# Performance work log

Hardware: AMD Instinct MI355X
Metric: run time of the kernel (lower is better)

## Reference

```python
import jax, jax.numpy as jnp
import numpy as np


def ternarize_weight(w):
    # abs-mean threshold quantization to {-am, 0, +am}
    abs_mean = jnp.maximum(jnp.abs(w).mean(), 1e-5)
    thr = 0.7 * abs_mean
    q = jnp.where(w > thr, 1.0, jnp.where(w < -thr, -1.0, 0.0))
    # STE: forward value is q*abs_mean, grad flows to w as identity
    return w + jax.lax.stop_gradient(q * abs_mean - w)


def rotate_half(x):
    x1, x2 = jnp.split(x, 2, axis=-1)
    return jnp.concatenate([-x2, x1], axis=-1)


def setup_inputs() -> dict:
    key = jax.random.key(0)
    k1, k2, k3, k4, k5 = jax.random.split(key, 5)
    B, T, C, H = 2, 2048, 1024, 16
    D = C // H
    x = jax.random.normal(k1, (B, T, C), dtype=jnp.float32)
    cos = jax.random.uniform(k2, (1, 1, T, D), dtype=jnp.float32)
    sin = jax.random.uniform(k3, (1, 1, T, D), dtype=jnp.float32)
    w_qkv = jax.random.normal(k4, (3 * C, C), dtype=jnp.float32) / np.sqrt(C)
    w_proj = jax.random.normal(k5, (C, C), dtype=jnp.float32) / np.sqrt(C)
    return {"x": x, "cos": cos, "sin": sin, "w_qkv": w_qkv, "w_proj": w_proj}


def reference(x, cos, sin, w_qkv, w_proj):
    B, T, C = x.shape
    H = 16
    D = C // H
    wq = ternarize_weight(w_qkv)
    wp = ternarize_weight(w_proj)
    qkv = x @ wq.T  # [B,T,3C]
    q, k, v = jnp.split(qkv, 3, axis=-1)
    # [B,T,C] -> [B,H,T,D]
    q = q.reshape(B, T, H, D).transpose(0, 2, 1, 3)
    k = k.reshape(B, T, H, D).transpose(0, 2, 1, 3)
    v = v.reshape(B, T, H, D).transpose(0, 2, 1, 3)
    # RoPE
    q = q * cos + rotate_half(q) * sin
    k = k * cos + rotate_half(k) * sin
    # causal SDPA
    scale = 1.0 / np.sqrt(D)
    scores = jnp.einsum("bhqd,bhkd->bhqk", q, k) * scale
    causal = jnp.tril(jnp.ones((T, T), dtype=bool))
    scores = jnp.where(causal, scores, jnp.finfo(scores.dtype).min)
    attn = jax.nn.softmax(scores, axis=-1)
    y = jnp.einsum("bhqk,bhkd->bhqd", attn, v)  # [B,H,T,D]
    y = y.transpose(0, 2, 1, 3).reshape(B, T, C)
    return y @ wp.T
```

## Files before the change

kernel.cpp:

```cpp
#include <hip/hip_runtime.h>
#include <hip/hip_bf16.h>

#define B_ 2
#define T_ 2048
#define C_ 1024
#define H_ 16
#define D_ 64
#define M_ 4096
#define N3C 3072

using short8  = __attribute__((ext_vector_type(8))) short;
using floatx4 = __attribute__((ext_vector_type(4))) float;
typedef unsigned int u32;

__device__ __forceinline__ unsigned short f2b(float f) {
  __hip_bfloat16 h = __float2bfloat16(f);
  return *reinterpret_cast<unsigned short*>(&h);
}
__device__ __forceinline__ float b2f(unsigned short u) {
  union { unsigned int i; float f; } x; x.i = ((unsigned int)u) << 16; return x.f;
}

__device__ __forceinline__ void gll16(const void* g, void* l) {
  __builtin_amdgcn_global_load_lds((const __attribute__((address_space(1))) u32*)g,
                                   (__attribute__((address_space(3))) u32*)l, 16, 0, 0);
}


__global__ void zero_sums(double* sums) {
  if (threadIdx.x < 2) sums[threadIdx.x] = 0.0;
}

__global__ void abs_sum_kernel(const float* __restrict__ w, int n4, double* out) {
  __shared__ double red[4];
  int stride = gridDim.x * blockDim.x;
  double s = 0.0;
  for (int i = blockIdx.x * blockDim.x + threadIdx.x; i < n4; i += stride) {
    float4 v = ((const float4*)w)[i];
    s += (double)fabsf(v.x) + (double)fabsf(v.y) + (double)fabsf(v.z) + (double)fabsf(v.w);
  }
  #pragma unroll
  for (int off = 32; off > 0; off >>= 1)
    s += __shfl_down(s, off, 64);
  if ((threadIdx.x & 63) == 0) red[threadIdx.x >> 6] = s;
  __syncthreads();
  if (threadIdx.x == 0) atomicAdd(out, (red[0] + red[1]) + (red[2] + red[3]));
}

__global__ void ternarize_all(const float* __restrict__ wq, const float* __restrict__ wp,
                              unsigned short* __restrict__ oq, unsigned short* __restrict__ op,
                              const double* __restrict__ sums, float* __restrict__ ams) {
  const int NQ = 3 * C_ * C_;
  const int NP = C_ * C_;
  int i = blockIdx.x * blockDim.x + threadIdx.x;
  float am0 = fmaxf((float)(sums[0] * (1.0 / NQ)), 1e-5f);
  float am1 = fmaxf((float)(sums[1] * (1.0 / NP)), 1e-5f);
  if (i == 0) { ams[0] = am0; ams[1] = am1; }
  if (i < NQ) {
    float thr = 0.7f * am0, x = wq[i];
    oq[i] = (x > thr) ? 0x3F80u : ((x < -thr) ? 0xBF80u : 0u);
  } else if (i < NQ + NP) {
    int j = i - NQ;
    float thr = 0.7f * am1, x = wp[j];
    op[j] = (x > thr) ? 0x3F80u : ((x < -thr) ? 0xBF80u : 0u);
  }
}

__global__ void cvt_f32_bf16(const float* __restrict__ in, unsigned short* __restrict__ out, int n4) {
  int i = blockIdx.x * blockDim.x + threadIdx.x;
  if (i < n4) {
    float4 v = ((const float4*)in)[i];
    ushort4 o; o.x = f2b(v.x); o.y = f2b(v.y); o.z = f2b(v.z); o.w = f2b(v.w);
    ((ushort4*)out)[i] = o;
  }
}


template<int OUT_BF16>
__global__ __launch_bounds__(256) void gemm128(const unsigned short* __restrict__ A,
                                               const unsigned short* __restrict__ W,
                                               const float* __restrict__ scale_ptr,
                                               void* __restrict__ Cout,
                                               int N, int K) {
  __shared__ __attribute__((aligned(16))) unsigned short As[128 * 32];
  __shared__ __attribute__((aligned(16))) unsigned short Ws[128 * 32];
  const int tid = threadIdx.x, lane = tid & 63, wv = tid >> 6;
  const int m = lane & 15, g = lane >> 4;
  const int m0 = blockIdx.y * 128, n0 = blockIdx.x * 128;
  const int wm = (wv >> 1) * 64, wn = (wv & 1) * 64;

  const int srow = wv * 16 + (lane >> 2);
  const int skoff = (lane & 3) * 8;
  const unsigned short* ga0 = A + (size_t)(m0 + srow) * K + skoff;
  const unsigned short* ga1 = A + (size_t)(m0 + 64 + srow) * K + skoff;
  const unsigned short* gw0 = W + (size_t)(n0 + srow) * K + skoff;
  const unsigned short* gw1 = W + (size_t)(n0 + 64 + srow) * K + skoff;
  unsigned short* la0 = As + (wv * 16) * 32;
  unsigned short* la1 = As + (64 + wv * 16) * 32;
  unsigned short* lw0 = Ws + (wv * 16) * 32;
  unsigned short* lw1 = Ws + (64 + wv * 16) * 32;

  floatx4 acc[4][4] = {};
  for (int kc = 0; kc < K; kc += 32) {
    __syncthreads();
    gll16(ga0, la0); gll16(ga1, la1); gll16(gw0, lw0); gll16(gw1, lw1);
    ga0 += 32; ga1 += 32; gw0 += 32; gw1 += 32;
    __syncthreads();
    short8 af[4], wf[4];
    #pragma unroll
    for (int r = 0; r < 4; r++)
      af[r] = *(const short8*)&As[(wm + r * 16 + m) * 32 + g * 8];
    #pragma unroll
    for (int c = 0; c < 4; c++)
      wf[c] = *(const short8*)&Ws[(wn + c * 16 + m) * 32 + g * 8];
    #pragma unroll
    for (int r = 0; r < 4; r++)
      #pragma unroll
      for (int c = 0; c < 4; c++)
        acc[r][c] = __builtin_amdgcn_mfma_f32_16x16x32_bf16(af[r], wf[c], acc[r][c], 0, 0, 0);
  }

  const float scale = *scale_ptr;
  #pragma unroll
  for (int r = 0; r < 4; r++)
    #pragma unroll
    for (int c = 0; c < 4; c++)
      #pragma unroll
      for (int i = 0; i < 4; i++) {
        int row = m0 + wm + r * 16 + g * 4 + i;
        int col = n0 + wn + c * 16 + m;
        float val = acc[r][c][i] * scale;
        if (OUT_BF16) ((unsigned short*)Cout)[(size_t)row * N + col] = f2b(val);
        else          ((float*)Cout)[(size_t)row * N + col] = val;
      }
}


__global__ __launch_bounds__(256) void rope_vtrans(const unsigned short* __restrict__ qkv,
                                                   const float* __restrict__ cosp,
                                                   const float* __restrict__ sinp,
                                                   unsigned short* __restrict__ Qb,
                                                   unsigned short* __restrict__ Kb,
                                                   unsigned short* __restrict__ Vtb) {
  __shared__ unsigned short L[64][65];
  const float QSC = 0.125f * 1.44269504088896340736f;
  const int bh = blockIdx.y, t0 = blockIdx.x * 64;
  const int b = bh >> 4, h = bh & 15;
  const size_t hb = (size_t)bh * T_ * 64;
  #pragma unroll
  for (int it = 0; it < 8; it++) {
    int idx = it * 256 + threadIdx.x;
    int tl = idx >> 5, p = idx & 31, t = t0 + tl;
    size_t rb = (size_t)(b * T_ + t) * N3C + h * 64;
    float q1 = b2f(qkv[rb + p]),      q2 = b2f(qkv[rb + p + 32]);
    float k1 = b2f(qkv[rb + C_ + p]), k2 = b2f(qkv[rb + C_ + p + 32]);
    float c1 = cosp[t * 64 + p], c2 = cosp[t * 64 + p + 32];
    float s1 = sinp[t * 64 + p], s2 = sinp[t * 64 + p + 32];
    size_t ob = hb + (size_t)t * 64;
    Qb[ob + p]      = f2b((q1 * c1 - q2 * s1) * QSC);
    Qb[ob + p + 32] = f2b((q2 * c2 + q1 * s2) * QSC);
    Kb[ob + p]      = f2b(k1 * c1 - k2 * s1);
    Kb[ob + p + 32] = f2b(k2 * c2 + k1 * s2);
  }
  #pragma unroll
  for (int it = 0; it < 16; it++) {
    int idx = it * 256 + threadIdx.x;
    int tl = idx >> 6, d = idx & 63;
    L[tl][d] = qkv[(size_t)(b * T_ + t0 + tl) * N3C + 2 * C_ + h * 64 + d];
  }
  __syncthreads();
  #pragma unroll
  for (int it = 0; it < 16; it++) {
    int idx = it * 256 + threadIdx.x;
    int dr = idx >> 6, tl = idx & 63;
    Vtb[hb + (size_t)dr * T_ + t0 + tl] = L[tl][dr];
  }
}


__global__ __launch_bounds__(256) void flash_mfma(const unsigned short* __restrict__ Qb,
                                                  const unsigned short* __restrict__ Kb,
                                                  const unsigned short* __restrict__ Vtb,
                                                  unsigned short* __restrict__ Y) {
  __shared__ __align__(16) unsigned short Ktile[2][64][64];
  __shared__ __align__(16) unsigned short Vtile[2][64][64];
  __shared__ __align__(16) unsigned short Plds[4][16][72];
  const int lane = threadIdx.x & 63;
  const int wv = threadIdx.x >> 6;
  const int m = lane & 15, g = lane >> 4;
  const int gid = blockIdx.x;
  const int xcd = gid & 7, idx = gid >> 3;
  const int bh = xcd * 4 + (idx >> 3);
  const int pr = idx & 7;
  const int b = bh >> 4, h = bh & 15;
  const size_t hb = (size_t)bh * T_ * 64;
  const unsigned short* Kbh = Kb + hb;
  const unsigned short* Vbh = Vtb + hb;
  const int r8 = lane >> 3, cc8 = lane & 7;
  const int gcol = ((cc8 ^ r8) << 3);

  #pragma unroll
  for (int sp = 0; sp < 2; sp++) {
    const int s = sp ? (15 - pr) : pr;
    const int ntiles = 2 * s + 2;
    const int qb0 = s * 128 + wv * 32;
    const int qb1 = qb0 + 16;

    const unsigned short* qp0 = Qb + hb + (size_t)(qb0 + m) * 64 + g * 8;
    short8 qf00 = *(const short8*)qp0;
    short8 qf01 = *(const short8*)(qp0 + 32);
    const unsigned short* qp1 = qp0 + 16 * 64;
    short8 qf10 = *(const short8*)qp1;
    short8 qf11 = *(const short8*)(qp1 + 32);

    floatx4 O0[4] = {}, O1[4] = {};
    float ls0 = 0.f, ls1 = 0.f;

    if (sp) __syncthreads();
    #pragma unroll
    for (int cc = 0; cc < 2; cc++) {
      int row = wv * 16 + cc * 8;
      gll16(Kbh + (size_t)(row + r8) * 64 + gcol, &Ktile[0][row][0]);
      gll16(Vbh + (size_t)(row + r8) * T_ + gcol, &Vtile[0][row][0]);
    }

    for (int kt = 0; kt < ntiles; kt++) {
      const int buf = kt & 1;
      const int kb = kt * 64;
      __syncthreads();
      if (kt + 1 < ntiles) {
        const int kb2 = kb + 64;
        #pragma unroll
        for (int cc = 0; cc < 2; cc++) {
          int row = wv * 16 + cc * 8;
          gll16(Kbh + (size_t)(kb2 + row + r8) * 64 + gcol, &Ktile[1 - buf][row][0]);
          gll16(Vbh + (size_t)(row + r8) * T_ + kb2 + gcol, &Vtile[1 - buf][row][0]);
        }
      }
      if (kb > qb0 + 31) continue;

      auto do_qset = [&](short8 qa, short8 qb_, int qbase, float& lsum, floatx4* O) {
        floatx4 S[4];
        #pragma unroll
        for (int mt = 0; mt < 4; mt++) {
          int row = mt * 16 + m;
          short8 kf0 = *(const short8*)&Ktile[buf][row][(g ^ (m & 7)) << 3];
          short8 kf1 = *(const short8*)&Ktile[buf][row][((g + 4) ^ (m & 7)) << 3];
          floatx4 sv = {};
          sv = __builtin_amdgcn_mfma_f32_16x16x32_bf16(kf0, qa, sv, 0, 0, 0);
          sv = __builtin_amdgcn_mfma_f32_16x16x32_bf16(kf1, qb_, sv, 0, 0, 0);
          S[mt] = sv;
        }
        if (kb + 64 <= qbase) {
          #pragma unroll
          for (int mt = 0; mt < 4; mt++) {
            float e0 = exp2f(S[mt][0]), e1 = exp2f(S[mt][1]);
            float e2 = exp2f(S[mt][2]), e3 = exp2f(S[mt][3]);
            lsum += (e0 + e1) + (e2 + e3);
            ushort4 o; o.x = f2b(e0); o.y = f2b(e1); o.z = f2b(e2); o.w = f2b(e3);
            *(ushort4*)&Plds[wv][m][mt * 16 + g * 4] = o;
          }
        } else {
          const int q_glob = qbase + m;
          #pragma unroll
          for (int mt = 0; mt < 4; mt++) {
            float e[4];
            #pragma unroll
            for (int r = 0; r < 4; r++) {
              int kg = kb + mt * 16 + g * 4 + r;
              e[r] = (kg <= q_glob) ? exp2f(S[mt][r]) : 0.f;
            }
            lsum += (e[0] + e[1]) + (e[2] + e[3]);
            ushort4 o; o.x = f2b(e[0]); o.y = f2b(e[1]); o.z = f2b(e[2]); o.w = f2b(e[3]);
            *(ushort4*)&Plds[wv][m][mt * 16 + g * 4] = o;
          }
        }
        short8 pa0 = *(const short8*)&Plds[wv][m][g * 8];
        short8 pa1 = *(const short8*)&Plds[wv][m][32 + g * 8];
        #pragma unroll
        for (int nt = 0; nt < 4; nt++) {
          int row = nt * 16 + m;
          short8 v0 = *(const short8*)&Vtile[buf][row][(g ^ (m & 7)) << 3];
          short8 v1 = *(const short8*)&Vtile[buf][row][((g + 4) ^ (m & 7)) << 3];
          O[nt] = __builtin_amdgcn_mfma_f32_16x16x32_bf16(pa0, v0, O[nt], 0, 0, 0);
          O[nt] = __builtin_amdgcn_mfma_f32_16x16x32_bf16(pa1, v1, O[nt], 0, 0, 0);
        }
      };

      do_qset(qf00, qf01, qb0, ls0, O0);
      if (kb <= qb1 + 15) do_qset(qf10, qf11, qb1, ls1, O1);
    }

    #pragma unroll
    for (int j = 0; j < 2; j++) {
      float lsum = j ? ls1 : ls0;
      floatx4* O = j ? O1 : O0;
      const int qbase = j ? qb1 : qb0;
      lsum += __shfl_xor(lsum, 16, 64);
      lsum += __shfl_xor(lsum, 32, 64);
      float li[4];
      #pragma unroll
      for (int r = 0; r < 4; r++) li[r] = 1.0f / __shfl(lsum, g * 4 + r, 64);
      #pragma unroll
      for (int nt = 0; nt < 4; nt++)
        #pragma unroll
        for (int r = 0; r < 4; r++) {
          int trow = qbase + g * 4 + r;
          int col = h * 64 + nt * 16 + m;
          Y[(size_t)(b * T_ + trow) * C_ + col] = f2b(O[nt][r] * li[r]);
        }
    }
  }
}


extern "C" void kernel_launch(void* const* d_in, const int* in_sizes, int n_in,
                              void* d_out, int out_size, void* d_ws, size_t ws_size,
                              hipStream_t stream) {
  (void)in_sizes; (void)n_in; (void)out_size; (void)ws_size;
  const float* x      = (const float*)d_in[0];
  const float* cosp   = (const float*)d_in[1];
  const float* sinp   = (const float*)d_in[2];
  const float* w_qkv  = (const float*)d_in[3];
  const float* w_proj = (const float*)d_in[4];
  float* out = (float*)d_out;

  char* ws = (char*)d_ws;
  double* sums = (double*)ws;
  float*  ams  = (float*)(ws + 16);
  unsigned short* wqkv_b  = (unsigned short*)(ws + 256);
  unsigned short* wproj_b = wqkv_b + (size_t)N3C * C_;
  unsigned short* xb      = wproj_b + (size_t)C_ * C_;
  unsigned short* qkv_b   = xb + (size_t)M_ * C_;
  unsigned short* Qb      = qkv_b + (size_t)M_ * N3C;
  unsigned short* Kb      = Qb + (size_t)B_ * H_ * T_ * D_;
  unsigned short* Vtb     = Kb + (size_t)B_ * H_ * T_ * D_;
  unsigned short* yb      = Vtb + (size_t)B_ * H_ * T_ * D_;

  zero_sums<<<1, 64, 0, stream>>>(sums);
  abs_sum_kernel<<<256, 256, 0, stream>>>(w_qkv, (3 * C_ * C_) / 4, sums + 0);
  abs_sum_kernel<<<128, 256, 0, stream>>>(w_proj, (C_ * C_) / 4, sums + 1);
  ternarize_all<<<(4 * C_ * C_) / 256, 256, 0, stream>>>(w_qkv, w_proj, wqkv_b, wproj_b,
                                                         sums, ams);
  cvt_f32_bf16<<<(M_ * C_ / 4 + 255) / 256, 256, 0, stream>>>(x, xb, M_ * C_ / 4);
  gemm128<1><<<dim3(N3C / 128, M_ / 128), 256, 0, stream>>>(xb, wqkv_b, ams + 0, qkv_b, N3C, C_);
  rope_vtrans<<<dim3(T_ / 64, B_ * H_), 256, 0, stream>>>(qkv_b, cosp, sinp, Qb, Kb, Vtb);
  flash_mfma<<<256, 256, 0, stream>>>(Qb, Kb, Vtb, yb);
  gemm128<0><<<dim3(C_ / 128, M_ / 128), 256, 0, stream>>>(yb, wproj_b, ams + 1, out, C_, C_);
}
```

Before: 224.3 us.

## Fuse RoPE into QKV GEMM epilogue, merge abs-sum launches, and re-split flash blocks

The QKV GEMM epilogue now applies RoPE and scaling and writes Q, K and V directly in head-major layout, which removes the separate qkv round trip through memory. The old rope kernel is reduced to a V transpose only. The two abs-sum launches become one 2D launch. Flash attention now runs 512 blocks that each handle one 64-row query tile per wave set with paired causal tiles, where before each block handled two 16-row q-sets per wave. This raises parallelism but drops the per-wave double q-set reuse of K/V tiles.

```diff
diff --git a/kernel.cpp b/kernel.cpp
--- a/kernel.cpp
+++ b/kernel.cpp
@@ -31,8 +31,11 @@
   if (threadIdx.x < 2) sums[threadIdx.x] = 0.0;
 }
 
-__global__ void abs_sum_kernel(const float* __restrict__ w, int n4, double* out) {
+__global__ void abs_sum2(const float* __restrict__ wq, const float* __restrict__ wp,
+                         double* __restrict__ sums) {
   __shared__ double red[4];
+  const float* w = blockIdx.y ? wp : wq;
+  const int n4 = blockIdx.y ? (C_ * C_ / 4) : (3 * C_ * C_ / 4);
   int stride = gridDim.x * blockDim.x;
   double s = 0.0;
   for (int i = blockIdx.x * blockDim.x + threadIdx.x; i < n4; i += stride) {
@@ -44,7 +47,7 @@
     s += __shfl_down(s, off, 64);
   if ((threadIdx.x & 63) == 0) red[threadIdx.x >> 6] = s;
   __syncthreads();
-  if (threadIdx.x == 0) atomicAdd(out, (red[0] + red[1]) + (red[2] + red[3]));
+  if (threadIdx.x == 0) atomicAdd(sums + blockIdx.y, (red[0] + red[1]) + (red[2] + red[3]));
 }
 
 __global__ void ternarize_all(const float* __restrict__ wq, const float* __restrict__ wp,
@@ -76,12 +79,15 @@
 }
 
 
-template<int OUT_BF16>
-__global__ __launch_bounds__(256) void gemm128(const unsigned short* __restrict__ A,
-                                               const unsigned short* __restrict__ W,
-                                               const float* __restrict__ scale_ptr,
-                                               void* __restrict__ Cout,
-                                               int N, int K) {
+__global__ __launch_bounds__(256) void gemm_qkv(const unsigned short* __restrict__ A,
+                                                const unsigned short* __restrict__ W,
+                                                const float* __restrict__ scale_ptr,
+                                                const float* __restrict__ cosp,
+                                                const float* __restrict__ sinp,
+                                                unsigned short* __restrict__ Qb,
+                                                unsigned short* __restrict__ Kb,
+                                                unsigned short* __restrict__ Vb) {
+  const int K = C_;
   __shared__ __attribute__((aligned(16))) unsigned short As[128 * 32];
   __shared__ __attribute__((aligned(16))) unsigned short Ws[128 * 32];
   const int tid = threadIdx.x, lane = tid & 63, wv = tid >> 6;
@@ -120,6 +126,88 @@
         acc[r][c] = __builtin_amdgcn_mfma_f32_16x16x32_bf16(af[r], wf[c], acc[r][c], 0, 0, 0);
   }
 
+  const float am = *scale_ptr;
+  const int sect = n0 >> 10;
+  const int nloc = n0 & 1023;
+  const int h = (nloc + wn) >> 6;
+  if (sect < 2) {
+    unsigned short* dst = sect ? Kb : Qb;
+    const float sc = sect ? am : am * 0.18033688011112042f;
+    #pragma unroll
+    for (int r = 0; r < 4; r++)
+      #pragma unroll
+      for (int i = 0; i < 4; i++) {
+        int row = m0 + wm + r * 16 + g * 4 + i;
+        int t = row & (T_ - 1), b = row >> 11;
+        size_t obase = ((size_t)(b * H_ + h) * T_ + t) * 64;
+        #pragma unroll
+        for (int c = 0; c < 4; c++) {
+          int p = c * 16 + m;
+          float cv = cosp[t * 64 + p], sv = sinp[t * 64 + p];
+          float a = acc[r][c][i], pt = acc[r][c ^ 2][i];
+          float val = (c < 2) ? (a * cv - pt * sv) : (a * cv + pt * sv);
+          dst[obase + p] = f2b(val * sc);
+        }
+      }
+  } else {
+    #pragma unroll
+    for (int r = 0; r < 4; r++)
+      #pragma unroll
+      for (int i = 0; i < 4; i++) {
+        int row = m0 + wm + r * 16 + g * 4 + i;
+        int t = row & (T_ - 1), b = row >> 11;
+        size_t obase = ((size_t)(b * H_ + h) * T_ + t) * 64;
+        #pragma unroll
+        for (int c = 0; c < 4; c++)
+          Vb[obase + c * 16 + m] = f2b(acc[r][c][i] * am);
+      }
+  }
+}
+
+
+__global__ __launch_bounds__(256) void gemm128(const unsigned short* __restrict__ A,
+                                               const unsigned short* __restrict__ W,
+                                               const float* __restrict__ scale_ptr,
+                                               float* __restrict__ Cout,
+                                               int N, int K) {
+  __shared__ __attribute__((aligned(16))) unsigned short As[128 * 32];
+  __shared__ __attribute__((aligned(16))) unsigned short Ws[128 * 32];
+  const int tid = threadIdx.x, lane = tid & 63, wv = tid >> 6;
+  const int m = lane & 15, g = lane >> 4;
+  const int m0 = blockIdx.y * 128, n0 = blockIdx.x * 128;
+  const int wm = (wv >> 1) * 64, wn = (wv & 1) * 64;
+
+  const int srow = wv * 16 + (lane >> 2);
+  const int skoff = (lane & 3) * 8;
+  const unsigned short* ga0 = A + (size_t)(m0 + srow) * K + skoff;
+  const unsigned short* ga1 = A + (size_t)(m0 + 64 + srow) * K + skoff;
+  const unsigned short* gw0 = W + (size_t)(n0 + srow) * K + skoff;
+  const unsigned short* gw1 = W + (size_t)(n0 + 64 + srow) * K + skoff;
+  unsigned short* la0 = As + (wv * 16) * 32;
+  unsigned short* la1 = As + (64 + wv * 16) * 32;
+  unsigned short* lw0 = Ws + (wv * 16) * 32;
+  unsigned short* lw1 = Ws + (64 + wv * 16) * 32;
+
+  floatx4 acc[4][4] = {};
+  for (int kc = 0; kc < K; kc += 32) {
+    __syncthreads();
+    gll16(ga0, la0); gll16(ga1, la1); gll16(gw0, lw0); gll16(gw1, lw1);
+    ga0 += 32; ga1 += 32; gw0 += 32; gw1 += 32;
+    __syncthreads();
+    short8 af[4], wf[4];
+    #pragma unroll
+    for (int r = 0; r < 4; r++)
+      af[r] = *(const short8*)&As[(wm + r * 16 + m) * 32 + g * 8];
+    #pragma unroll
+    for (int c = 0; c < 4; c++)
+      wf[c] = *(const short8*)&Ws[(wn + c * 16 + m) * 32 + g * 8];
+    #pragma unroll
+    for (int r = 0; r < 4; r++)
+      #pragma unroll
+      for (int c = 0; c < 4; c++)
+        acc[r][c] = __builtin_amdgcn_mfma_f32_16x16x32_bf16(af[r], wf[c], acc[r][c], 0, 0, 0);
+  }
+
   const float scale = *scale_ptr;
   #pragma unroll
   for (int r = 0; r < 4; r++)
@@ -129,44 +217,21 @@
       for (int i = 0; i < 4; i++) {
         int row = m0 + wm + r * 16 + g * 4 + i;
         int col = n0 + wn + c * 16 + m;
-        float val = acc[r][c][i] * scale;
-        if (OUT_BF16) ((unsigned short*)Cout)[(size_t)row * N + col] = f2b(val);
-        else          ((float*)Cout)[(size_t)row * N + col] = val;
-      }
-}
-
-
-__global__ __launch_bounds__(256) void rope_vtrans(const unsigned short* __restrict__ qkv,
-                                                   const float* __restrict__ cosp,
-                                                   const float* __restrict__ sinp,
-                                                   unsigned short* __restrict__ Qb,
-                                                   unsigned short* __restrict__ Kb,
+        Cout[(size_t)row * N + col] = acc[r][c][i] * scale;
+      }
+}
+
+
+__global__ __launch_bounds__(256) void v_transpose(const unsigned short* __restrict__ Vb,
                                                    unsigned short* __restrict__ Vtb) {
   __shared__ unsigned short L[64][65];
-  const float QSC = 0.125f * 1.44269504088896340736f;
   const int bh = blockIdx.y, t0 = blockIdx.x * 64;
-  const int b = bh >> 4, h = bh & 15;
   const size_t hb = (size_t)bh * T_ * 64;
-  #pragma unroll
-  for (int it = 0; it < 8; it++) {
-    int idx = it * 256 + threadIdx.x;
-    int tl = idx >> 5, p = idx & 31, t = t0 + tl;
-    size_t rb = (size_t)(b * T_ + t) * N3C + h * 64;
-    float q1 = b2f(qkv[rb + p]),      q2 = b2f(qkv[rb + p + 32]);
-    float k1 = b2f(qkv[rb + C_ + p]), k2 = b2f(qkv[rb + C_ + p + 32]);
-    float c1 = cosp[t * 64 + p], c2 = cosp[t * 64 + p + 32];
-    float s1 = sinp[t * 64 + p], s2 = sinp[t * 64 + p + 32];
-    size_t ob = hb + (size_t)t * 64;
-    Qb[ob + p]      = f2b((q1 * c1 - q2 * s1) * QSC);
-    Qb[ob + p + 32] = f2b((q2 * c2 + q1 * s2) * QSC);
-    Kb[ob + p]      = f2b(k1 * c1 - k2 * s1);
-    Kb[ob + p + 32] = f2b(k2 * c2 + k1 * s2);
-  }
   #pragma unroll
   for (int it = 0; it < 16; it++) {
     int idx = it * 256 + threadIdx.x;
     int tl = idx >> 6, d = idx & 63;
-    L[tl][d] = qkv[(size_t)(b * T_ + t0 + tl) * N3C + 2 * C_ + h * 64 + d];
+    L[tl][d] = Vb[hb + (size_t)(t0 + tl) * 64 + d];
   }
   __syncthreads();
   #pragma unroll
@@ -189,9 +254,9 @@
   const int wv = threadIdx.x >> 6;
   const int m = lane & 15, g = lane >> 4;
   const int gid = blockIdx.x;
-  const int xcd = gid & 7, idx = gid >> 3;
-  const int bh = xcd * 4 + (idx >> 3);
-  const int pr = idx & 7;
+  const int xcd = gid & 7, j = gid >> 3;
+  const int bh = xcd * 4 + (j >> 4);
+  const int pr = j & 15;
   const int b = bh >> 4, h = bh & 15;
   const size_t hb = (size_t)bh * T_ * 64;
   const unsigned short* Kbh = Kb + hb;
@@ -201,20 +266,17 @@
 
   #pragma unroll
   for (int sp = 0; sp < 2; sp++) {
-    const int s = sp ? (15 - pr) : pr;
-    const int ntiles = 2 * s + 2;
-    const int qb0 = s * 128 + wv * 32;
-    const int qb1 = qb0 + 16;
-
-    const unsigned short* qp0 = Qb + hb + (size_t)(qb0 + m) * 64 + g * 8;
-    short8 qf00 = *(const short8*)qp0;
-    short8 qf01 = *(const short8*)(qp0 + 32);
-    const unsigned short* qp1 = qp0 + 16 * 64;
-    short8 qf10 = *(const short8*)qp1;
-    short8 qf11 = *(const short8*)(qp1 + 32);
-
-    floatx4 O0[4] = {}, O1[4] = {};
-    float ls0 = 0.f, ls1 = 0.f;
+    const int s = sp ? pr : (31 - pr);
+    const int qbase = s * 64 + wv * 16;
+    const int q_glob = qbase + m;
+    const int ntiles = s + 1;
+
+    const unsigned short* qp = Qb + hb + (size_t)(qbase + m) * 64 + g * 8;
+    short8 qf0 = *(const short8*)qp;
+    short8 qf1 = *(const short8*)(qp + 32);
+
+    floatx4 O[4] = {};
+    float lsum = 0.f;
 
     if (sp) __syncthreads();
     #pragma unroll
@@ -237,79 +299,65 @@
           gll16(Vbh + (size_t)(row + r8) * T_ + kb2 + gcol, &Vtile[1 - buf][row][0]);
         }
       }
-      if (kb > qb0 + 31) continue;
-
-      auto do_qset = [&](short8 qa, short8 qb_, int qbase, float& lsum, floatx4* O) {
-        floatx4 S[4];
+      floatx4 S[4];
+      #pragma unroll
+      for (int mt = 0; mt < 4; mt++) {
+        int row = mt * 16 + m;
+        short8 kf0 = *(const short8*)&Ktile[buf][row][(g ^ (m & 7)) << 3];
+        short8 kf1 = *(const short8*)&Ktile[buf][row][((g + 4) ^ (m & 7)) << 3];
+        floatx4 sv = {};
+        sv = __builtin_amdgcn_mfma_f32_16x16x32_bf16(kf0, qf0, sv, 0, 0, 0);
+        sv = __builtin_amdgcn_mfma_f32_16x16x32_bf16(kf1, qf1, sv, 0, 0, 0);
+        S[mt] = sv;
+      }
+      if (kt + 1 < ntiles) {
         #pragma unroll
         for (int mt = 0; mt < 4; mt++) {
-          int row = mt * 16 + m;
-          short8 kf0 = *(const short8*)&Ktile[buf][row][(g ^ (m & 7)) << 3];
-          short8 kf1 = *(const short8*)&Ktile[buf][row][((g + 4) ^ (m & 7)) << 3];
-          floatx4 sv = {};
-          sv = __builtin_amdgcn_mfma_f32_16x16x32_bf16(kf0, qa, sv, 0, 0, 0);
-          sv = __builtin_amdgcn_mfma_f32_16x16x32_bf16(kf1, qb_, sv, 0, 0, 0);
-          S[mt] = sv;
+          float e0 = exp2f(S[mt][0]), e1 = exp2f(S[mt][1]);
+          float e2 = exp2f(S[mt][2]), e3 = exp2f(S[mt][3]);
+          lsum += (e0 + e1) + (e2 + e3);
+          ushort4 o; o.x = f2b(e0); o.y = f2b(e1); o.z = f2b(e2); o.w = f2b(e3);
+          *(ushort4*)&Plds[wv][m][mt * 16 + g * 4] = o;
         }
-        if (kb + 64 <= qbase) {
+      } else {
+        #pragma unroll
+        for (int mt = 0; mt < 4; mt++) {
+          float e[4];
           #pragma unroll
-          for (int mt = 0; mt < 4; mt++) {
-            float e0 = exp2f(S[mt][0]), e1 = exp2f(S[mt][1]);
-            float e2 = exp2f(S[mt][2]), e3 = exp2f(S[mt][3]);
-            lsum += (e0 + e1) + (e2 + e3);
-            ushort4 o; o.x = f2b(e0); o.y = f2b(e1); o.z = f2b(e2); o.w = f2b(e3);
-            *(ushort4*)&Plds[wv][m][mt * 16 + g * 4] = o;
+          for (int r = 0; r < 4; r++) {
+            int kg = kb + mt * 16 + g * 4 + r;
+            e[r] = (kg <= q_glob) ? exp2f(S[mt][r]) : 0.f;
           }
-        } else {
-          const int q_glob = qbase + m;
-          #pragma unroll
-          for (int mt = 0; mt < 4; mt++) {
-            float e[4];
-            #pragma unroll
-            for (int r = 0; r < 4; r++) {
-              int kg = kb + mt * 16 + g * 4 + r;
-              e[r] = (kg <= q_glob) ? exp2f(S[mt][r]) : 0.f;
-            }
-            lsum += (e[0] + e[1]) + (e[2] + e[3]);
-            ushort4 o; o.x = f2b(e[0]); o.y = f2b(e[1]); o.z = f2b(e[2]); o.w = f2b(e[3]);
-            *(ushort4*)&Plds[wv][m][mt * 16 + g * 4] = o;
-          }
+          lsum += (e[0] + e[1]) + (e[2] + e[3]);
+          ushort4 o; o.x = f2b(e[0]); o.y = f2b(e[1]); o.z = f2b(e[2]); o.w = f2b(e[3]);
+          *(ushort4*)&Plds[wv][m][mt * 16 + g * 4] = o;
         }
-        short8 pa0 = *(const short8*)&Plds[wv][m][g * 8];
-        short8 pa1 = *(const short8*)&Plds[wv][m][32 + g * 8];
-        #pragma unroll
-        for (int nt = 0; nt < 4; nt++) {
-          int row = nt * 16 + m;
-          short8 v0 = *(const short8*)&Vtile[buf][row][(g ^ (m & 7)) << 3];
-          short8 v1 = *(const short8*)&Vtile[buf][row][((g + 4) ^ (m & 7)) << 3];
-          O[nt] = __builtin_amdgcn_mfma_f32_16x16x32_bf16(pa0, v0, O[nt], 0, 0, 0);
-          O[nt] = __builtin_amdgcn_mfma_f32_16x16x32_bf16(pa1, v1, O[nt], 0, 0, 0);
-        }
-      };
-
-      do_qset(qf00, qf01, qb0, ls0, O0);
-      if (kb <= qb1 + 15) do_qset(qf10, qf11, qb1, ls1, O1);
+      }
+      short8 pa0 = *(const short8*)&Plds[wv][m][g * 8];
+      short8 pa1 = *(const short8*)&Plds[wv][m][32 + g * 8];
+      #pragma unroll
+      for (int nt = 0; nt < 4; nt++) {
+        int row = nt * 16 + m;
+        short8 v0 = *(const short8*)&Vtile[buf][row][(g ^ (m & 7)) << 3];
+        short8 v1 = *(const short8*)&Vtile[buf][row][((g + 4) ^ (m & 7)) << 3];
+        O[nt] = __builtin_amdgcn_mfma_f32_16x16x32_bf16(pa0, v0, O[nt], 0, 0, 0);
+        O[nt] = __builtin_amdgcn_mfma_f32_16x16x32_bf16(pa1, v1, O[nt], 0, 0, 0);
+      }
     }
 
-    #pragma unroll
-    for (int j = 0; j < 2; j++) {
-      float lsum = j ? ls1 : ls0;
-      floatx4* O = j ? O1 : O0;
-      const int qbase = j ? qb1 : qb0;
-      lsum += __shfl_xor(lsum, 16, 64);
-      lsum += __shfl_xor(lsum, 32, 64);
-      float li[4];
-      #pragma unroll
-      for (int r = 0; r < 4; r++) li[r] = 1.0f / __shfl(lsum, g * 4 + r, 64);
-      #pragma unroll
-      for (int nt = 0; nt < 4; nt++)
-        #pragma unroll
-        for (int r = 0; r < 4; r++) {
-          int trow = qbase + g * 4 + r;
-          int col = h * 64 + nt * 16 + m;
-          Y[(size_t)(b * T_ + trow) * C_ + col] = f2b(O[nt][r] * li[r]);
-        }
-    }
+    lsum += __shfl_xor(lsum, 16, 64);
+    lsum += __shfl_xor(lsum, 32, 64);
+    float li[4];
+    #pragma unroll
+    for (int r = 0; r < 4; r++) li[r] = 1.0f / __shfl(lsum, g * 4 + r, 64);
+    #pragma unroll
+    for (int nt = 0; nt < 4; nt++)
+      #pragma unroll
+      for (int r = 0; r < 4; r++) {
+        int trow = qbase + g * 4 + r;
+        int col = h * 64 + nt * 16 + m;
+        Y[(size_t)(b * T_ + trow) * C_ + col] = f2b(O[nt][r] * li[r]);
+      }
   }
 }
 
@@ -331,20 +379,20 @@
   unsigned short* wqkv_b  = (unsigned short*)(ws + 256);
   unsigned short* wproj_b = wqkv_b + (size_t)N3C * C_;
   unsigned short* xb      = wproj_b + (size_t)C_ * C_;
-  unsigned short* qkv_b   = xb + (size_t)M_ * C_;
-  unsigned short* Qb      = qkv_b + (size_t)M_ * N3C;
+  unsigned short* Qb      = xb + (size_t)M_ * C_;
   unsigned short* Kb      = Qb + (size_t)B_ * H_ * T_ * D_;
-  unsigned short* Vtb     = Kb + (size_t)B_ * H_ * T_ * D_;
+  unsigned short* Vb      = Kb + (size_t)B_ * H_ * T_ * D_;
+  unsigned short* Vtb     = Vb + (size_t)B_ * H_ * T_ * D_;
   unsigned short* yb      = Vtb + (size_t)B_ * H_ * T_ * D_;
 
   zero_sums<<<1, 64, 0, stream>>>(sums);
-  abs_sum_kernel<<<256, 256, 0, stream>>>(w_qkv, (3 * C_ * C_) / 4, sums + 0);
-  abs_sum_kernel<<<128, 256, 0, stream>>>(w_proj, (C_ * C_) / 4, sums + 1);
+  abs_sum2<<<dim3(256, 2), 256, 0, stream>>>(w_qkv, w_proj, sums);
   ternarize_all<<<(4 * C_ * C_) / 256, 256, 0, stream>>>(w_qkv, w_proj, wqkv_b, wproj_b,
                                                          sums, ams);
   cvt_f32_bf16<<<(M_ * C_ / 4 + 255) / 256, 256, 0, stream>>>(x, xb, M_ * C_ / 4);
-  gemm128<1><<<dim3(N3C / 128, M_ / 128), 256, 0, stream>>>(xb, wqkv_b, ams + 0, qkv_b, N3C, C_);
-  rope_vtrans<<<dim3(T_ / 64, B_ * H_), 256, 0, stream>>>(qkv_b, cosp, sinp, Qb, Kb, Vtb);
-  flash_mfma<<<256, 256, 0, stream>>>(Qb, Kb, Vtb, yb);
-  gemm128<0><<<dim3(C_ / 128, M_ / 128), 256, 0, stream>>>(yb, wproj_b, ams + 1, out, C_, C_);
-}
+  gemm_qkv<<<dim3(N3C / 128, M_ / 128), 256, 0, stream>>>(xb, wqkv_b, ams + 0,
+                                                          cosp, sinp, Qb, Kb, Vb);
+  v_transpose<<<dim3(T_ / 64, B_ * H_), 256, 0, stream>>>(Vb, Vtb);
+  flash_mfma<<<512, 256, 0, stream>>>(Qb, Kb, Vtb, yb);
+  gemm128<<<dim3(C_ / 128, M_ / 128), 256, 0, stream>>>(yb, wproj_b, ams + 1, out, C_, C_);
+}
```

Measured after the change: 225.5 us. Within noise of the previous version (+0.5%).
